# Kernel tuning notes

Hardware: AMD Instinct MI355X
Metric: run time of the kernel (lower is better)

## Reference

```python
import jax, jax.numpy as jnp
import numpy as np

E, D_IN, D_OUT, RANK, ALPHA = 8, 2048, 2048, 8, 8.0
SCALING = ALPHA / RANK


def setup_inputs() -> dict:
    key = jax.random.key(0)
    ks = jax.random.split(key, 7)
    x = jax.random.normal(ks[0], (2, 4096, D_IN), dtype=jnp.float32)
    # base linear fc: weight [d_out, d_in], bias [d_out]
    Wf = jax.random.normal(ks[1], (D_OUT, D_IN), dtype=jnp.float32) / np.sqrt(D_IN)
    bf = jax.random.normal(ks[2], (D_OUT,), dtype=jnp.float32) * 0.01
    # router: weight [E, d_in], bias [E]
    Wr = jax.random.normal(ks[3], (E, D_IN), dtype=jnp.float32) / np.sqrt(D_IN)
    br = jnp.zeros((E,), dtype=jnp.float32)
    # stacked LoRA factors: A [E, rank, d_in] (kaiming-uniform-like), B [E, d_out, rank]
    # (original inits lora_B to zeros; use small random values so grads are non-trivial)
    A = jax.random.uniform(ks[4], (E, RANK, D_IN), dtype=jnp.float32,
                           minval=-1.0, maxval=1.0) / np.sqrt(D_IN)
    Bm = jax.random.normal(ks[5], (E, D_OUT, RANK), dtype=jnp.float32) * 0.02
    return {"x": x, "Wf": Wf, "bf": bf, "Wr": Wr, "br": br, "A": A, "Bm": Bm}


def reference(x, Wf, bf, Wr, br, A, Bm):
    # base output: x @ Wf^T + bf  -> [B, T, d_out]
    base = jnp.einsum('btd,od->bto', x, Wf) + bf
    # router softmax over experts -> [B, T, E]
    logits = jnp.einsum('btd,ed->bte', x, Wr) + br
    w = jax.nn.softmax(logits, axis=-1)
    # all-expert low-rank projection: h = x @ A_e^T -> [B, T, E, rank]
    h = jnp.einsum('btd,erd->bter', x, A)
    # up-project and fuse routing-weighted accumulation -> [B, T, d_out]
    lora = SCALING * jnp.einsum('bter,eor,bte->bto', h, Bm, w)
    return base + lora, w
```

## Files before the change

### kernel.cpp

```cpp
#include <hip/hip_runtime.h>
#include <hip/hip_bf16.h>

#define BT      8192
#define DIN     2048
#define DOUT    2048
#define NEXP    8
#define RANK    8
#define KX      2112
#define NSPLIT  4
#define HLD     72
#define SCALING 1.0f
#define SLOT    32768

typedef __bf16 bf16x8 __attribute__((ext_vector_type(8)));
typedef __bf16 bf16x4 __attribute__((ext_vector_type(4)));
typedef float  f32x4  __attribute__((ext_vector_type(4)));

#define XB_OFF     0
#define XB_BYTES   (BT * KX * 2)
#define WB_OFF     (XB_OFF + XB_BYTES)
#define WB_BYTES   (DOUT * KX * 2)
#define ACAT_OFF   (WB_OFF + WB_BYTES)
#define ACAT_BYTES (128 * DIN * 2)
#define HP_OFF     (ACAT_OFF + ACAT_BYTES)
#define HP_BYTES   (NSPLIT * BT * HLD * 4)

__device__ __forceinline__ void gload_lds16(const void* g, void* l) {
    __builtin_amdgcn_global_load_lds(
        (__attribute__((address_space(1))) void*)(g),
        (__attribute__((address_space(3))) void*)(l),
        16, 0, 0);
}

#define MFMA16(a, b, c) __builtin_amdgcn_mfma_f32_16x16x32_bf16((a), (b), (c), 0, 0, 0)

__global__ __launch_bounds__(256) void mole_prep(
    const float* __restrict__ Wf, const float* __restrict__ Bm,
    const float* __restrict__ Wr, const float* __restrict__ A,
    __bf16* __restrict__ WB, __bf16* __restrict__ ACAT)
{
    const int i = blockIdx.x * 256 + threadIdx.x;
    const int R1 = DOUT * (DIN / 4);
    const int R2 = DOUT * 64;
    if (i < R1) {
        const int o = i >> 9, c4 = i & 511;
        float4 v = ((const float4*)Wf)[(size_t)o * 512 + c4];
        bf16x4 b; b[0] = (__bf16)v.x; b[1] = (__bf16)v.y; b[2] = (__bf16)v.z; b[3] = (__bf16)v.w;
        *(bf16x4*)&WB[(size_t)o * KX + (c4 << 2)] = b;
    } else if (i < R1 + R2) {
        const int j = i - R1;
        const int o = j >> 6, c = j & 63;
        const int e = c >> 3, r = c & 7;
        WB[(size_t)o * KX + DIN + c] = (__bf16)Bm[((size_t)e * DOUT + o) * RANK + r];
    } else {
        const int j = i - (R1 + R2);
        const int r = j >> 9, c4 = j & 511;
        float4 v;
        if (r < 8)        v = ((const float4*)Wr)[(size_t)r * 512 + c4];
        else if (r < 72)  v = ((const float4*)A)[(size_t)(r - 8) * 512 + c4];
        else              v = make_float4(0.f, 0.f, 0.f, 0.f);
        bf16x4 b; b[0] = (__bf16)v.x; b[1] = (__bf16)v.y; b[2] = (__bf16)v.z; b[3] = (__bf16)v.w;
        *(bf16x4*)&ACAT[(size_t)r * DIN + (c4 << 2)] = b;
    }
}

__global__ __launch_bounds__(256) void mole_hconv(
    const float* __restrict__ x, const __bf16* __restrict__ ACAT,
    __bf16* __restrict__ XB, float* __restrict__ HP)
{
    __shared__ __align__(16) __bf16 Xs[128][32];
    __shared__ __align__(16) __bf16 Bs[128][32];

    const int tid = threadIdx.x;
    const int wv  = tid >> 6, ln = tid & 63;
    const int wr  = wv >> 1, wc = wv & 1;
    const size_t m0 = (size_t)blockIdx.x * 128;
    const int kStart = blockIdx.z * (DIN / NSPLIT);
    float* C = HP + (size_t)blockIdx.z * BT * HLD;

    const int xr = tid >> 3;
    const int xc = (tid & 7) << 2;
    const float* gx  = x  + (m0 + xr) * (size_t)DIN + kStart + xc;
    __bf16*      gxb = XB + (m0 + xr) * (size_t)KX  + kStart + xc;

    const int srow = (wv << 4) + (ln >> 2);
    const int scol = (ln & 3) << 3;
    const __bf16* gB0 = ACAT + srow * (size_t)DIN + kStart + scol;
    const __bf16* gB1 = gB0 + (size_t)64 * DIN;
    __bf16* lB0 = &Bs[(wv << 4)][0];
    __bf16* lB1 = &Bs[64 + (wv << 4)][0];

    f32x4 acc[4][4] = {};
    const int fr = ln & 15;
    const int fk = (ln >> 4) << 3;

    for (int ks = 0; ks < (DIN / NSPLIT) / 32; ++ks) {
        gload_lds16(gB0, lB0);
        gload_lds16(gB1, lB1);
        gB0 += 32; gB1 += 32;
        #pragma unroll
        for (int j = 0; j < 4; ++j) {
            float4 v = *(const float4*)(gx + (size_t)(32 * j) * DIN + 32 * ks);
            bf16x4 b; b[0] = (__bf16)v.x; b[1] = (__bf16)v.y;
            b[2] = (__bf16)v.z; b[3] = (__bf16)v.w;
            *(bf16x4*)&Xs[xr + 32 * j][xc] = b;
            *(bf16x4*)(gxb + (size_t)(32 * j) * KX + 32 * ks) = b;
        }
        __syncthreads();

        bf16x8 af[4], bfr[4];
        #pragma unroll
        for (int m = 0; m < 4; ++m)
            af[m] = *(const bf16x8*)&Xs[(wr << 6) + (m << 4) + fr][fk];
        #pragma unroll
        for (int n = 0; n < 4; ++n)
            bfr[n] = *(const bf16x8*)&Bs[(wc << 6) + (n << 4) + fr][fk];
        #pragma unroll
        for (int m = 0; m < 4; ++m)
            #pragma unroll
            for (int n = 0; n < 4; ++n)
                acc[m][n] = MFMA16(af[m], bfr[n], acc[m][n]);
        __syncthreads();
    }

    const int cr = (ln >> 4) << 2;
    const int cc = ln & 15;
    #pragma unroll
    for (int n = 0; n < 4; ++n) {
        const int col = (wc << 6) + (n << 4) + cc;
        if (col < HLD) {
            #pragma unroll
            for (int m = 0; m < 4; ++m) {
                const size_t row = m0 + (wr << 6) + (m << 4) + cr;
                #pragma unroll
                for (int r = 0; r < 4; ++r)
                    C[(row + r) * (size_t)HLD + col] = acc[m][n][r];
            }
        }
    }
}

__global__ __launch_bounds__(256) void mole_softmax_g(
    const float* __restrict__ HP, const float* __restrict__ br,
    float* __restrict__ wOut, __bf16* __restrict__ XB)
{
    const int t   = blockIdx.x * 4 + (threadIdx.x >> 6);
    const int tid = threadIdx.x & 63;
    float h = 0.0f;
    #pragma unroll
    for (int sp = 0; sp < NSPLIT; ++sp)
        h += HP[((size_t)sp * BT + t) * HLD + 8 + tid];

    float lg[NEXP];
    #pragma unroll
    for (int e = 0; e < NEXP; ++e) {
        lg[e] = br[e];
        #pragma unroll
        for (int sp = 0; sp < NSPLIT; ++sp)
            lg[e] += HP[((size_t)sp * BT + t) * HLD + e];
    }
    float mx = lg[0];
    #pragma unroll
    for (int e = 1; e < NEXP; ++e) mx = fmaxf(mx, lg[e]);
    float ex[NEXP], den = 0.0f;
    #pragma unroll
    for (int e = 0; e < NEXP; ++e) { ex[e] = expf(lg[e] - mx); den += ex[e]; }

    const float w_my = ex[tid >> 3] / den;
    XB[(size_t)t * KX + DIN + tid] = (__bf16)(SCALING * w_my * h);
    if (tid < NEXP) wOut[(size_t)t * NEXP + tid] = ex[tid] / den;
}

__global__ __launch_bounds__(512, 1) void mole_gemm256(
    const __bf16* __restrict__ XBp, const __bf16* __restrict__ WBp,
    float* __restrict__ C, const float* __restrict__ bias)
{
    __shared__ __align__(16) char smem[131072];

    const int tid = threadIdx.x;
    const int wv  = tid >> 6, l = tid & 63;
    const int wm  = wv >> 2, wn = wv & 3;
    const int bid = blockIdx.x;
    const int xcd = bid & 7, ib = bid >> 3;
    const int tm = xcd * 4 + (ib & 3), tn = ib >> 2;
    const size_t m0 = (size_t)tm * 256, n0 = (size_t)tn * 256;

    const int op = wv >> 2, ww = wv & 3;
    const __bf16* gstage = (op == 0 ? XBp + (m0 + ww * 64) * KX
                                    : WBp + (n0 + ww * 64) * KX)
                         + (size_t)(l >> 2) * KX + (((l & 3) ^ ((l >> 3) & 3)) << 3);
    const int stageBase = op * 16384 + ww * 4096;

    const int fr = l & 15, fq = l >> 4;
    const int swz = (fq ^ ((fr >> 1) & 3)) << 4;
    const int aByte = (wm * 128 + fr) * 64 + swz;
    const int bByte = 16384 + (wn * 64 + fr) * 64 + swz;

    f32x4 acc[8][4] = {};
    bf16x8 fa0[8], fb0[4], fa1[8], fb1[4];

#define STAGE(S)                                                              \
    {                                                                         \
        char* dst = smem + ((S) & 3) * SLOT + stageBase;                      \
        const __bf16* g = gstage + (size_t)(S) * 32;                          \
        _Pragma("unroll")                                                     \
        for (int j = 0; j < 4; ++j)                                           \
            gload_lds16(g + (size_t)j * 16 * KX, dst + j * 1024);             \
    }

#define READS(S, FA, FB)                                                      \
    {                                                                         \
        const char* slot = smem + ((S) & 3) * SLOT;                           \
        _Pragma("unroll")                                                     \
        for (int nf = 0; nf < 4; ++nf)                                        \
            FB[nf] = *(const bf16x8*)(slot + bByte + nf * 1024);              \
        _Pragma("unroll")                                                     \
        for (int mf = 0; mf < 8; ++mf)                                        \
            FA[mf] = *(const bf16x8*)(slot + aByte + mf * 1024);              \
    }

#define STEP(S, VMN, DOSTAGE, DOREAD, FAc, FBc, FAn, FBn)                     \
    {                                                                         \
        asm volatile("s_waitcnt vmcnt(" #VMN ")" ::: "memory");               \
        __builtin_amdgcn_s_barrier();                                         \
        if (DOREAD) READS((S) + 1, FAn, FBn);                                 \
        if (DOSTAGE) STAGE((S) + 3);                                          \
        __builtin_amdgcn_sched_barrier(0);                                    \
        __builtin_amdgcn_s_setprio(1);                                        \
        _Pragma("unroll")                                                     \
        for (int mf = 0; mf < 8; ++mf)                                        \
            _Pragma("unroll")                                                 \
            for (int nf = 0; nf < 4; ++nf)                                    \
                acc[mf][nf] = MFMA16(FAc[mf], FBc[nf], acc[mf][nf]);          \
        __builtin_amdgcn_s_setprio(0);                                        \
    }

    STAGE(0); STAGE(1); STAGE(2);
    asm volatile("s_waitcnt vmcnt(8)" ::: "memory");
    __builtin_amdgcn_s_barrier();
    READS(0, fa0, fb0);

    #pragma unroll 1
    for (int s = 0; s < 62; s += 2) {
        STEP(s,     4, true, true, fa0, fb0, fa1, fb1);
        STEP(s + 1, 4, true, true, fa1, fb1, fa0, fb0);
    }
    STEP(62, 4, true,  true,  fa0, fb0, fa1, fb1);
    STEP(63, 4, false, true,  fa1, fb1, fa0, fb0);
    STEP(64, 0, false, true,  fa0, fb0, fa1, fb1);
    STEP(65, 0, false, false, fa1, fb1, fa0, fb0);
#undef STEP
#undef READS
#undef STAGE

    const size_t crow = m0 + wm * 128 + fq * 4;
    const size_t ccol = n0 + wn * 64 + fr;
    #pragma unroll
    for (int nf = 0; nf < 4; ++nf) {
        const float bv = bias[ccol + nf * 16];
        #pragma unroll
        for (int mf = 0; mf < 8; ++mf) {
            float* cp = C + (crow + (size_t)mf * 16) * DOUT + ccol + nf * 16;
            #pragma unroll
            for (int i = 0; i < 4; ++i)
                cp[(size_t)i * DOUT] = acc[mf][nf][i] + bv;
        }
    }
}

extern "C" void kernel_launch(void* const* d_in, const int* in_sizes, int n_in,
                              void* d_out, int out_size, void* d_ws, size_t ws_size,
                              hipStream_t stream) {
    const float* x  = (const float*)d_in[0];
    const float* Wf = (const float*)d_in[1];
    const float* bf = (const float*)d_in[2];
    const float* Wr = (const float*)d_in[3];
    const float* br = (const float*)d_in[4];
    const float* A  = (const float*)d_in[5];
    const float* Bm = (const float*)d_in[6];

    float* out0 = (float*)d_out;
    float* wOut = out0 + (size_t)BT * DOUT;

    char* ws = (char*)d_ws;
    __bf16* XB   = (__bf16*)(ws + XB_OFF);
    __bf16* WB   = (__bf16*)(ws + WB_OFF);
    __bf16* ACAT = (__bf16*)(ws + ACAT_OFF);
    float*  HP   = (float*)(ws + HP_OFF);

    mole_prep<<<4864, 256, 0, stream>>>(Wf, Bm, Wr, A, WB, ACAT);
    mole_hconv<<<dim3(64, 1, NSPLIT), 256, 0, stream>>>(x, ACAT, XB, HP);
    mole_softmax_g<<<BT / 4, 256, 0, stream>>>(HP, br, wOut, XB);
    mole_gemm256<<<256, 512, 0, stream>>>(XB, WB, out0, bf);
}
```

Before: 103.5 us.

## Use 4-wave 256x256 GEMM tiles with 128x128 per-wave outputs, drop register double-buffer

The GEMM block drops from 8 waves to 4, so each wave now computes a 128x128 output sub-tile (8x8 MFMA fragments) instead of 128x64. This raises the MFMA work per LDS fragment read. The explicit register double-buffering of the A/B fragments is replaced with a single load of the fragments per step, and each wave now stages both the A and B tiles. The trade-off is much higher register pressure (64 accumulator vectors) and less latency hiding from fewer waves and no register prefetch.

```diff
diff --git a/kernel.cpp b/kernel.cpp
--- a/kernel.cpp
+++ b/kernel.cpp
@@ -7,6 +7,7 @@
 #define NEXP    8
 #define RANK    8
 #define KX      2112
+#define NSUB    66
 #define NSPLIT  4
 #define HLD     72
 #define SCALING 1.0f
@@ -171,7 +172,7 @@
     if (tid < NEXP) wOut[(size_t)t * NEXP + tid] = ex[tid] / den;
 }
 
-__global__ __launch_bounds__(512, 1) void mole_gemm256(
+__global__ __launch_bounds__(256, 1) void mole_gemm256(
     const __bf16* __restrict__ XBp, const __bf16* __restrict__ WBp,
     float* __restrict__ C, const float* __restrict__ bias)
 {
@@ -179,84 +180,76 @@
 
     const int tid = threadIdx.x;
     const int wv  = tid >> 6, l = tid & 63;
-    const int wm  = wv >> 2, wn = wv & 3;
+    const int wm  = wv >> 1, wn = wv & 1;
     const int bid = blockIdx.x;
     const int xcd = bid & 7, ib = bid >> 3;
     const int tm = xcd * 4 + (ib & 3), tn = ib >> 2;
     const size_t m0 = (size_t)tm * 256, n0 = (size_t)tn * 256;
 
-    const int op = wv >> 2, ww = wv & 3;
-    const __bf16* gstage = (op == 0 ? XBp + (m0 + ww * 64) * KX
-                                    : WBp + (n0 + ww * 64) * KX)
-                         + (size_t)(l >> 2) * KX + (((l & 3) ^ ((l >> 3) & 3)) << 3);
-    const int stageBase = op * 16384 + ww * 4096;
+    const int swcol = ((l & 3) ^ ((l >> 3) & 3)) << 3;
+    const __bf16* gsA = XBp + (m0 + 64 * wv + (l >> 2)) * (size_t)KX + swcol;
+    const __bf16* gsB = WBp + (n0 + 64 * wv + (l >> 2)) * (size_t)KX + swcol;
+    const int dA = wv * 4096;
+    const int dB = 16384 + wv * 4096;
 
     const int fr = l & 15, fq = l >> 4;
     const int swz = (fq ^ ((fr >> 1) & 3)) << 4;
     const int aByte = (wm * 128 + fr) * 64 + swz;
-    const int bByte = 16384 + (wn * 64 + fr) * 64 + swz;
-
-    f32x4 acc[8][4] = {};
-    bf16x8 fa0[8], fb0[4], fa1[8], fb1[4];
+    const int bByte = 16384 + (wn * 128 + fr) * 64 + swz;
+
+    f32x4 acc[8][8] = {};
 
 #define STAGE(S)                                                              \
     {                                                                         \
-        char* dst = smem + ((S) & 3) * SLOT + stageBase;                      \
-        const __bf16* g = gstage + (size_t)(S) * 32;                          \
+        char* base = smem + ((S) & 3) * SLOT;                                 \
+        const __bf16* gA_ = gsA + (size_t)(S) * 32;                           \
+        const __bf16* gB_ = gsB + (size_t)(S) * 32;                           \
         _Pragma("unroll")                                                     \
         for (int j = 0; j < 4; ++j)                                           \
-            gload_lds16(g + (size_t)j * 16 * KX, dst + j * 1024);             \
-    }
-
-#define READS(S, FA, FB)                                                      \
-    {                                                                         \
-        const char* slot = smem + ((S) & 3) * SLOT;                           \
-        _Pragma("unroll")                                                     \
-        for (int nf = 0; nf < 4; ++nf)                                        \
-            FB[nf] = *(const bf16x8*)(slot + bByte + nf * 1024);              \
-        _Pragma("unroll")                                                     \
-        for (int mf = 0; mf < 8; ++mf)                                        \
-            FA[mf] = *(const bf16x8*)(slot + aByte + mf * 1024);              \
-    }
-
-#define STEP(S, VMN, DOSTAGE, DOREAD, FAc, FBc, FAn, FBn)                     \
+            gload_lds16(gA_ + (size_t)j * 16 * KX, base + dA + j * 1024);     \
+        _Pragma("unroll")                                                     \
+        for (int j = 0; j < 4; ++j)                                           \
+            gload_lds16(gB_ + (size_t)j * 16 * KX, base + dB + j * 1024);     \
+    }
+
+#define STEP(S, VMN, DOSTAGE)                                                 \
     {                                                                         \
         asm volatile("s_waitcnt vmcnt(" #VMN ")" ::: "memory");               \
         __builtin_amdgcn_s_barrier();                                         \
-        if (DOREAD) READS((S) + 1, FAn, FBn);                                 \
+        const char* slot = smem + ((S) & 3) * SLOT;                           \
+        bf16x8 fa[8], fb[8];                                                  \
+        _Pragma("unroll")                                                     \
+        for (int nf = 0; nf < 8; ++nf)                                        \
+            fb[nf] = *(const bf16x8*)(slot + bByte + nf * 1024);              \
+        _Pragma("unroll")                                                     \
+        for (int mf = 0; mf < 8; ++mf)                                        \
+            fa[mf] = *(const bf16x8*)(slot + aByte + mf * 1024);              \
         if (DOSTAGE) STAGE((S) + 3);                                          \
         __builtin_amdgcn_sched_barrier(0);                                    \
         __builtin_amdgcn_s_setprio(1);                                        \
         _Pragma("unroll")                                                     \
         for (int mf = 0; mf < 8; ++mf)                                        \
             _Pragma("unroll")                                                 \
-            for (int nf = 0; nf < 4; ++nf)                                    \
-                acc[mf][nf] = MFMA16(FAc[mf], FBc[nf], acc[mf][nf]);          \
+            for (int nf = 0; nf < 8; ++nf)                                    \
+                acc[mf][nf] = MFMA16(fa[mf], fb[nf], acc[mf][nf]);            \
         __builtin_amdgcn_s_setprio(0);                                        \
     }
 
     STAGE(0); STAGE(1); STAGE(2);
-    asm volatile("s_waitcnt vmcnt(8)" ::: "memory");
-    __builtin_amdgcn_s_barrier();
-    READS(0, fa0, fb0);
 
     #pragma unroll 1
-    for (int s = 0; s < 62; s += 2) {
-        STEP(s,     4, true, true, fa0, fb0, fa1, fb1);
-        STEP(s + 1, 4, true, true, fa1, fb1, fa0, fb0);
-    }
-    STEP(62, 4, true,  true,  fa0, fb0, fa1, fb1);
-    STEP(63, 4, false, true,  fa1, fb1, fa0, fb0);
-    STEP(64, 0, false, true,  fa0, fb0, fa1, fb1);
-    STEP(65, 0, false, false, fa1, fb1, fa0, fb0);
+    for (int s = 0; s < NSUB - 3; ++s)
+        STEP(s, 16, true);
+    STEP(NSUB - 3, 16, false);
+    STEP(NSUB - 2, 8,  false);
+    STEP(NSUB - 1, 0,  false);
 #undef STEP
-#undef READS
 #undef STAGE
 
     const size_t crow = m0 + wm * 128 + fq * 4;
-    const size_t ccol = n0 + wn * 64 + fr;
-    #pragma unroll
-    for (int nf = 0; nf < 4; ++nf) {
+    const size_t ccol = n0 + wn * 128 + fr;
+    #pragma unroll
+    for (int nf = 0; nf < 8; ++nf) {
         const float bv = bias[ccol + nf * 16];
         #pragma unroll
         for (int mf = 0; mf < 8; ++mf) {
@@ -291,5 +284,5 @@
     mole_prep<<<4864, 256, 0, stream>>>(Wf, Bm, Wr, A, WB, ACAT);
     mole_hconv<<<dim3(64, 1, NSPLIT), 256, 0, stream>>>(x, ACAT, XB, HP);
     mole_softmax_g<<<BT / 4, 256, 0, stream>>>(HP, br, wOut, XB);
-    mole_gemm256<<<256, 512, 0, stream>>>(XB, WB, out0, bf);
-}
+    mole_gemm256<<<256, 256, 0, stream>>>(XB, WB, out0, bf);
+}
```

Result: slower. 111.0 us (+7.3%).

## Load GEMM B fragments directly from global into registers, stage only A in LDS

Applied to the files above, without the earlier changes.

The 256x256 GEMM now stages only the activation (A) tile through LDS with async global-to-LDS loads, while each wave loads its weight (B) fragments straight from global memory into registers, one k-step ahead. LDS use halves and the vmcnt waits are adjusted for the new per-step load count. A fragments are now read from LDS at the start of each step rather than prefetched a step early. The aim is to cut LDS traffic and footprint. In exchange, B global-load latency is exposed with only one step of lookahead, two waves fetch the same B rows redundantly, and A LDS reads are no longer hidden behind the previous step's MFMAs.

```diff
diff --git a/kernel.cpp b/kernel.cpp
--- a/kernel.cpp
+++ b/kernel.cpp
@@ -7,10 +7,11 @@
 #define NEXP    8
 #define RANK    8
 #define KX      2112
+#define NSUB    66
 #define NSPLIT  4
 #define HLD     72
 #define SCALING 1.0f
-#define SLOT    32768
+#define SLOTA   16384
 
 typedef __bf16 bf16x8 __attribute__((ext_vector_type(8)));
 typedef __bf16 bf16x4 __attribute__((ext_vector_type(4)));
@@ -175,7 +176,7 @@
     const __bf16* __restrict__ XBp, const __bf16* __restrict__ WBp,
     float* __restrict__ C, const float* __restrict__ bias)
 {
-    __shared__ __align__(16) char smem[131072];
+    __shared__ __align__(16) char smem[65536];
 
     const int tid = threadIdx.x;
     const int wv  = tid >> 6, l = tid & 63;
@@ -185,73 +186,73 @@
     const int tm = xcd * 4 + (ib & 3), tn = ib >> 2;
     const size_t m0 = (size_t)tm * 256, n0 = (size_t)tn * 256;
 
-    const int op = wv >> 2, ww = wv & 3;
-    const __bf16* gstage = (op == 0 ? XBp + (m0 + ww * 64) * KX
-                                    : WBp + (n0 + ww * 64) * KX)
-                         + (size_t)(l >> 2) * KX + (((l & 3) ^ ((l >> 3) & 3)) << 3);
-    const int stageBase = op * 16384 + ww * 4096;
+    const int swcol = ((l & 3) ^ ((l >> 3) & 3)) << 3;
+    const __bf16* gsA = XBp + (m0 + 32 * wv + (l >> 2)) * (size_t)KX + swcol;
+    const int dA = wv * 2048;
+
+    const __bf16* gBf = WBp + (n0 + wn * 64 + (l & 15)) * (size_t)KX + ((l >> 4) << 3);
 
     const int fr = l & 15, fq = l >> 4;
     const int swz = (fq ^ ((fr >> 1) & 3)) << 4;
     const int aByte = (wm * 128 + fr) * 64 + swz;
-    const int bByte = 16384 + (wn * 64 + fr) * 64 + swz;
 
     f32x4 acc[8][4] = {};
-    bf16x8 fa0[8], fb0[4], fa1[8], fb1[4];
-
-#define STAGE(S)                                                              \
+    bf16x8 fbg0[4], fbg1[4];
+
+#define STAGEA(S)                                                             \
     {                                                                         \
-        char* dst = smem + ((S) & 3) * SLOT + stageBase;                      \
-        const __bf16* g = gstage + (size_t)(S) * 32;                          \
-        _Pragma("unroll")                                                     \
-        for (int j = 0; j < 4; ++j)                                           \
-            gload_lds16(g + (size_t)j * 16 * KX, dst + j * 1024);             \
-    }
-
-#define READS(S, FA, FB)                                                      \
+        char* dst = smem + ((S) & 3) * SLOTA + dA;                            \
+        const __bf16* g = gsA + (size_t)(S) * 32;                             \
+        gload_lds16(g, dst);                                                  \
+        gload_lds16(g + (size_t)16 * KX, dst + 1024);                         \
+    }
+
+#define LOADB(S, FB)                                                          \
     {                                                                         \
-        const char* slot = smem + ((S) & 3) * SLOT;                           \
         _Pragma("unroll")                                                     \
         for (int nf = 0; nf < 4; ++nf)                                        \
-            FB[nf] = *(const bf16x8*)(slot + bByte + nf * 1024);              \
-        _Pragma("unroll")                                                     \
-        for (int mf = 0; mf < 8; ++mf)                                        \
-            FA[mf] = *(const bf16x8*)(slot + aByte + mf * 1024);              \
-    }
-
-#define STEP(S, VMN, DOSTAGE, DOREAD, FAc, FBc, FAn, FBn)                     \
+            FB[nf] = *(const bf16x8*)(gBf + (size_t)nf * 16 * KX              \
+                                          + (size_t)(S) * 32);                \
+    }
+
+#define STEP(S, VMN, DOSTAGE, DOLOADB, FBc, FBn)                              \
     {                                                                         \
         asm volatile("s_waitcnt vmcnt(" #VMN ")" ::: "memory");               \
         __builtin_amdgcn_s_barrier();                                         \
-        if (DOREAD) READS((S) + 1, FAn, FBn);                                 \
-        if (DOSTAGE) STAGE((S) + 3);                                          \
+        const char* slot = smem + ((S) & 3) * SLOTA;                          \
+        bf16x8 fa[8];                                                         \
+        _Pragma("unroll")                                                     \
+        for (int mf = 0; mf < 8; ++mf)                                        \
+            fa[mf] = *(const bf16x8*)(slot + aByte + mf * 1024);              \
+        if (DOLOADB) LOADB((S) + 1, FBn);                                     \
+        if (DOSTAGE) STAGEA((S) + 3);                                         \
         __builtin_amdgcn_sched_barrier(0);                                    \
         __builtin_amdgcn_s_setprio(1);                                        \
         _Pragma("unroll")                                                     \
         for (int mf = 0; mf < 8; ++mf)                                        \
             _Pragma("unroll")                                                 \
             for (int nf = 0; nf < 4; ++nf)                                    \
-                acc[mf][nf] = MFMA16(FAc[mf], FBc[nf], acc[mf][nf]);          \
+                acc[mf][nf] = MFMA16(fa[mf], FBc[nf], acc[mf][nf]);           \
         __builtin_amdgcn_s_setprio(0);                                        \
     }
 
-    STAGE(0); STAGE(1); STAGE(2);
-    asm volatile("s_waitcnt vmcnt(8)" ::: "memory");
+    STAGEA(0); STAGEA(1); STAGEA(2);
+    LOADB(0, fbg0);
+    asm volatile("s_waitcnt vmcnt(0)" ::: "memory");
     __builtin_amdgcn_s_barrier();
-    READS(0, fa0, fb0);
 
     #pragma unroll 1
     for (int s = 0; s < 62; s += 2) {
-        STEP(s,     4, true, true, fa0, fb0, fa1, fb1);
-        STEP(s + 1, 4, true, true, fa1, fb1, fa0, fb0);
-    }
-    STEP(62, 4, true,  true,  fa0, fb0, fa1, fb1);
-    STEP(63, 4, false, true,  fa1, fb1, fa0, fb0);
-    STEP(64, 0, false, true,  fa0, fb0, fa1, fb1);
-    STEP(65, 0, false, false, fa1, fb1, fa0, fb0);
+        STEP(s,     2, true, true, fbg0, fbg1);
+        STEP(s + 1, 2, true, true, fbg1, fbg0);
+    }
+    STEP(62, 2, true,  true,  fbg0, fbg1);
+    STEP(63, 2, false, true,  fbg1, fbg0);
+    STEP(64, 0, false, true,  fbg0, fbg1);
+    STEP(65, 0, false, false, fbg1, fbg0);
 #undef STEP
-#undef READS
-#undef STAGE
+#undef LOADB
+#undef STAGEA
 
     const size_t crow = m0 + wm * 128 + fq * 4;
     const size_t ccol = n0 + wn * 64 + fr;
```

Result: slower. 135.8 us (+31.2%).

## Use five-slot LDS ring with one barrier per two K-substeps in GEMM

Applied to the files above, without the earlier changes.

The GEMM main loop moves from a 4-slot LDS ring with a barrier and vmcnt wait on every K substep to a 5-slot ring (160KB LDS) with one wait and barrier per pair of substeps. Fragment reads are no longer register double-buffered across steps; each substep loads its own fragments and then issues MFMAs. The aim is to cut barrier and wait overhead. In exchange, LDS-read latency is exposed before each MFMA batch, and the larger LDS footprint may affect occupancy or fail to fit.

```diff
diff --git a/kernel.cpp b/kernel.cpp
--- a/kernel.cpp
+++ b/kernel.cpp
@@ -7,10 +7,12 @@
 #define NEXP    8
 #define RANK    8
 #define KX      2112
+#define NSUB    66
 #define NSPLIT  4
 #define HLD     72
 #define SCALING 1.0f
 #define SLOT    32768
+#define LDSZ    163840
 
 typedef __bf16 bf16x8 __attribute__((ext_vector_type(8)));
 typedef __bf16 bf16x4 __attribute__((ext_vector_type(4)));
@@ -175,7 +177,7 @@
     const __bf16* __restrict__ XBp, const __bf16* __restrict__ WBp,
     float* __restrict__ C, const float* __restrict__ bias)
 {
-    __shared__ __align__(16) char smem[131072];
+    __shared__ __align__(16) char smem[LDSZ];
 
     const int tid = threadIdx.x;
     const int wv  = tid >> 6, l = tid & 63;
@@ -197,61 +199,72 @@
     const int bByte = 16384 + (wn * 64 + fr) * 64 + swz;
 
     f32x4 acc[8][4] = {};
-    bf16x8 fa0[8], fb0[4], fa1[8], fb1[4];
-
-#define STAGE(S)                                                              \
+
+#define STAGEAT(STB, GS)                                                      \
     {                                                                         \
-        char* dst = smem + ((S) & 3) * SLOT + stageBase;                      \
-        const __bf16* g = gstage + (size_t)(S) * 32;                          \
+        char* dst = smem + (STB) + stageBase;                                 \
         _Pragma("unroll")                                                     \
         for (int j = 0; j < 4; ++j)                                           \
-            gload_lds16(g + (size_t)j * 16 * KX, dst + j * 1024);             \
-    }
-
-#define READS(S, FA, FB)                                                      \
+            gload_lds16((GS) + (size_t)j * 16 * KX, dst + j * 1024);          \
+    }
+
+#define STEPBODY(SB, GS, DOSTAGE, STB)                                        \
     {                                                                         \
-        const char* slot = smem + ((S) & 3) * SLOT;                           \
+        const char* slot = smem + (SB);                                       \
+        bf16x8 fa[8], fb[4];                                                  \
         _Pragma("unroll")                                                     \
         for (int nf = 0; nf < 4; ++nf)                                        \
-            FB[nf] = *(const bf16x8*)(slot + bByte + nf * 1024);              \
+            fb[nf] = *(const bf16x8*)(slot + bByte + nf * 1024);              \
         _Pragma("unroll")                                                     \
         for (int mf = 0; mf < 8; ++mf)                                        \
-            FA[mf] = *(const bf16x8*)(slot + aByte + mf * 1024);              \
-    }
-
-#define STEP(S, VMN, DOSTAGE, DOREAD, FAc, FBc, FAn, FBn)                     \
-    {                                                                         \
-        asm volatile("s_waitcnt vmcnt(" #VMN ")" ::: "memory");               \
-        __builtin_amdgcn_s_barrier();                                         \
-        if (DOREAD) READS((S) + 1, FAn, FBn);                                 \
-        if (DOSTAGE) STAGE((S) + 3);                                          \
-        __builtin_amdgcn_sched_barrier(0);                                    \
+            fa[mf] = *(const bf16x8*)(slot + aByte + mf * 1024);              \
+        if (DOSTAGE) STAGEAT(STB, GS);                                        \
         __builtin_amdgcn_s_setprio(1);                                        \
         _Pragma("unroll")                                                     \
         for (int mf = 0; mf < 8; ++mf)                                        \
             _Pragma("unroll")                                                 \
             for (int nf = 0; nf < 4; ++nf)                                    \
-                acc[mf][nf] = MFMA16(FAc[mf], FBc[nf], acc[mf][nf]);          \
+                acc[mf][nf] = MFMA16(fa[mf], fb[nf], acc[mf][nf]);            \
         __builtin_amdgcn_s_setprio(0);                                        \
     }
 
-    STAGE(0); STAGE(1); STAGE(2);
-    asm volatile("s_waitcnt vmcnt(8)" ::: "memory");
-    __builtin_amdgcn_s_barrier();
-    READS(0, fa0, fb0);
+    STAGEAT(0 * SLOT, gstage + 0 * 32);
+    STAGEAT(1 * SLOT, gstage + 1 * 32);
+    STAGEAT(2 * SLOT, gstage + 2 * 32);
+
+    int sb = 0;
+    const __bf16* gsn = gstage + 96;
 
     #pragma unroll 1
     for (int s = 0; s < 62; s += 2) {
-        STEP(s,     4, true, true, fa0, fb0, fa1, fb1);
-        STEP(s + 1, 4, true, true, fa1, fb1, fa0, fb0);
-    }
-    STEP(62, 4, true,  true,  fa0, fb0, fa1, fb1);
-    STEP(63, 4, false, true,  fa1, fb1, fa0, fb0);
-    STEP(64, 0, false, true,  fa0, fb0, fa1, fb1);
-    STEP(65, 0, false, false, fa1, fb1, fa0, fb0);
-#undef STEP
-#undef READS
-#undef STAGE
+        asm volatile("s_waitcnt vmcnt(4)" ::: "memory");
+        __builtin_amdgcn_s_barrier();
+        int sb1 = sb + SLOT;     if (sb1 >= LDSZ) sb1 -= LDSZ;
+        int st0 = sb + 3 * SLOT; if (st0 >= LDSZ) st0 -= LDSZ;
+        int st1 = sb + 4 * SLOT; if (st1 >= LDSZ) st1 -= LDSZ;
+        STEPBODY(sb,  gsn,      1, st0);
+        STEPBODY(sb1, gsn + 32, 1, st1);
+        gsn += 64;
+        sb = sb1 + SLOT; if (sb >= LDSZ) sb -= LDSZ;
+    }
+    {
+        asm volatile("s_waitcnt vmcnt(4)" ::: "memory");
+        __builtin_amdgcn_s_barrier();
+        int sb1 = sb + SLOT;     if (sb1 >= LDSZ) sb1 -= LDSZ;
+        int st0 = sb + 3 * SLOT; if (st0 >= LDSZ) st0 -= LDSZ;
+        STEPBODY(sb,  gsn, 1, st0);
+        STEPBODY(sb1, gsn, 0, 0);
+        sb = sb1 + SLOT; if (sb >= LDSZ) sb -= LDSZ;
+    }
+    {
+        asm volatile("s_waitcnt vmcnt(0)" ::: "memory");
+        __builtin_amdgcn_s_barrier();
+        int sb1 = sb + SLOT;     if (sb1 >= LDSZ) sb1 -= LDSZ;
+        STEPBODY(sb,  gsn, 0, 0);
+        STEPBODY(sb1, gsn, 0, 0);
+    }
+#undef STEPBODY
+#undef STAGEAT
 
     const size_t crow = m0 + wm * 128 + fq * 4;
     const size_t ccol = n0 + wn * 64 + fr;
```

After: 103.0 us. About the same (-0.5%).
